# Kernel tuning notes

Measured on AMD Instinct MI355X. Metric: run time of the kernel, lower is better.

Reference implementation:

```python
import jax, jax.numpy as jnp
import numpy as np

NX, NQ, NU = 2048, 2048, 16
EPS = 0.01
STD = 0.5


def setup_inputs() -> dict:
    key = jax.random.key(0)
    ks = jax.random.split(key, 8)
    return {
        "t": 0,
        "x": jax.random.normal(ks[0], (NX,), dtype=jnp.float32),
        "u": jax.random.normal(ks[1], (NU,), dtype=jnp.float32),
        "X": jax.random.normal(ks[2], (NX + NQ, NX + NQ), dtype=jnp.float32) * STD,
        "U": jax.random.normal(ks[3], (NX, NQ), dtype=jnp.float32) * STD,
        "Y1": jax.random.normal(ks[4], (NX, NX), dtype=jnp.float32) * STD,
        "XP": jax.random.normal(ks[5], (NX, NX), dtype=jnp.float32) * STD,
        "B2": jax.random.normal(ks[6], (NX, NU), dtype=jnp.float32) * STD,
        "D12": jax.random.normal(ks[7], (NQ, NU), dtype=jnp.float32) * STD,
    }


def _constrained_mats(X, U, Y1, XP):
    nx = XP.shape[0]
    nq = U.shape[1]
    # P = XP XP^T + eps I ;  H = X X^T + eps I   (F.linear(A,B)=A@B.T)
    P = XP @ XP.T + EPS * jnp.eye(nx, dtype=XP.dtype)
    H = X @ X.T + EPS * jnp.eye(nx + nq, dtype=X.dtype)
    H11 = H[:nx, :nx]
    H12 = H[:nx, nx:]
    H22 = H[nx:, nx:]
    Y = -0.5 * (H11 + Y1 - Y1.T)
    Pinv = jnp.linalg.inv(P)
    A = Pinv @ Y                        # F.linear(inv(P), Y.T) = inv(P) @ Y
    lam = 0.5 * jnp.diagonal(H22)       # diagonal of Lambda
    D11 = -jnp.tril(H22, -1) / lam[:, None]   # strictly lower triangular
    C1 = U.T / lam[:, None]             # inv(Lambda) @ U.T
    B1 = Pinv @ (-H12 - U)
    return A, B1, C1, D11


def _solve_w(D11, c):
    nq = c.shape[0]

    def step(w, inp):
        i, d_row, ci = inp
        wi = jax.nn.relu(ci + jnp.dot(d_row, w))
        return w.at[i].set(wi), None

    w0 = jnp.zeros(nq, dtype=c.dtype)
    w, _ = jax.lax.scan(step, w0, (jnp.arange(nq), D11, c))
    return w


def reference(t, x, u, X, U, Y1, XP, B2, D12):
    A, B1, C1, D11 = _constrained_mats(X, U, Y1, XP)
    c = C1 @ x + D12 @ u                # precomputed affine part (bv = 0, bias=False)
    w = _solve_w(D11, c)
    x_dot = A @ x + B1 @ w + B2 @ u     # bx = 0
    return x_dot
```

## Files before the change

### kernel.cpp

```cpp
#include <hip/hip_runtime.h>
#include <math.h>

#define NQ2 2048
#define NT  4096
#define NUU 16
#define FEPS 0.01f
#define NB  64
#define NBLK 32
#define NSB 128
#define NSP 132
#define NSBLK 16
#define GCH 16

typedef __attribute__((ext_vector_type(8))) short short8;
typedef __attribute__((ext_vector_type(4))) float floatx4;

__device__ __forceinline__ float readlane_f(float v, int lane) {
  return __int_as_float(__builtin_amdgcn_readlane(__float_as_int(v), lane));
}
__device__ __forceinline__ unsigned short f2bf(float x) {
  unsigned u = __float_as_uint(x);
  unsigned r = u + 0x7FFFu + ((u >> 16) & 1u);
  return (unsigned short)(r >> 16);
}
__device__ __forceinline__ float bf2f(unsigned short h) {
  return __uint_as_float(((unsigned)h) << 16);
}

__device__ __forceinline__ float wave_reduce(float v) {
#pragma unroll
  for (int off = 32; off > 0; off >>= 1) v += __shfl_down(v, off, 64);
  return v;
}
__device__ __forceinline__ float block_reduce_256(float v) {
  __shared__ float sm[4];
  v = wave_reduce(v);
  if ((threadIdx.x & 63) == 0) sm[threadIdx.x >> 6] = v;
  __syncthreads();
  return (threadIdx.x == 0) ? (sm[0] + sm[1] + sm[2] + sm[3]) : 0.0f;
}

__global__ __launch_bounds__(256) void lam_kernel(const float* __restrict__ X,
                                                  float* __restrict__ invlam) {
  int row = blockIdx.x;
  const float* xr = X + (size_t)(NQ2 + row) * NT;
  float s = 0.f;
  for (int k = threadIdx.x * 4; k < NT; k += 1024) {
    float4 v = *(const float4*)(xr + k);
    s += v.x * v.x + v.y * v.y + v.z * v.z + v.w * v.w;
  }
  float tot = block_reduce_256(s);
  if (threadIdx.x == 0) invlam[row] = 1.0f / (0.5f * (tot + FEPS));
}

__global__ __launch_bounds__(256) void tgemv_part_kernel(const float* __restrict__ A,
                                                         const float* __restrict__ v,
                                                         float* __restrict__ part) {
  int col = blockIdx.x * 256 + threadIdx.x;
  int ch = blockIdx.y;
  int i0 = ch * (NQ2 / GCH), i1 = i0 + NQ2 / GCH;
  float s = 0.f;
#pragma unroll 4
  for (int i = i0; i < i1; i++) s = fmaf(A[(size_t)i * NQ2 + col], v[i], s);
  part[(size_t)ch * NQ2 + col] = s;
}

template <int FM>
__global__ __launch_bounds__(256) void finish_kernel(const float* __restrict__ part,
                                                     const float* __restrict__ invlam,
                                                     const float* __restrict__ D12,
                                                     const float* __restrict__ u,
                                                     float* __restrict__ dst) {
  int col = blockIdx.x * 256 + threadIdx.x;
  float s = 0.f;
#pragma unroll
  for (int ch = 0; ch < GCH; ch++) s += part[(size_t)ch * NQ2 + col];
  if (FM == 0) {
    float d = 0.f;
#pragma unroll
    for (int j = 0; j < NUU; j++) d += D12[(size_t)col * NUU + j] * u[j];
    dst[col] = s * invlam[col] + d;
  } else if (FM == 1) {
    dst[col] += 0.5f * s;
  } else {
    dst[col] = s;
  }
}

__device__ void syrk512_body(const float* __restrict__ A, int lda, int K,
                             float* __restrict__ C, float eps, int L, int tid) {
  __shared__ __align__(16) short Ah[4096], Al[4096], Bh[4096], Bl[4096];

  int bi = (int)((sqrtf(8.0f * (float)L + 1.0f) - 1.0f) * 0.5f);
  while ((bi + 1) * (bi + 2) / 2 <= L) bi++;
  while (bi * (bi + 1) / 2 > L) bi--;
  int bj = L - bi * (bi + 1) / 2;
  int row0 = bi * 128, col0 = bj * 128;

  int l = tid & 63;
  int w = tid >> 6;
  int wr = w >> 1, wc = w & 1;

  int g = tid;
  int ar = (g >> 6) * 16 + (g & 15), ak = ((g >> 4) & 3) * 8;
  const float* pa = A + (size_t)(row0 + ar) * lda + ak;
  const float* pb = A + (size_t)(col0 + ar) * lda + ak;

  floatx4 acc[4][4];
#pragma unroll
  for (int m = 0; m < 4; m++)
#pragma unroll
    for (int n = 0; n < 4; n++) acc[m][n] = (floatx4){0.f, 0.f, 0.f, 0.f};

  float xa[8], xb[8];
  {
    float4 t0 = *(const float4*)(pa), t1 = *(const float4*)(pa + 4);
    xa[0]=t0.x; xa[1]=t0.y; xa[2]=t0.z; xa[3]=t0.w; xa[4]=t1.x; xa[5]=t1.y; xa[6]=t1.z; xa[7]=t1.w;
    t0 = *(const float4*)(pb); t1 = *(const float4*)(pb + 4);
    xb[0]=t0.x; xb[1]=t0.y; xb[2]=t0.z; xb[3]=t0.w; xb[4]=t1.x; xb[5]=t1.y; xb[6]=t1.z; xb[7]=t1.w;
  }

  for (int k0 = 0; k0 < K; k0 += 32) {
    __syncthreads();
    {
      short8 h, lo;
#pragma unroll
      for (int j = 0; j < 8; j++) { unsigned short hb = f2bf(xa[j]); h[j] = (short)hb; lo[j] = (short)f2bf(xa[j] - bf2f(hb)); }
      *(short8*)&Ah[g * 8] = h; *(short8*)&Al[g * 8] = lo;
#pragma unroll
      for (int j = 0; j < 8; j++) { unsigned short hb = f2bf(xb[j]); h[j] = (short)hb; lo[j] = (short)f2bf(xb[j] - bf2f(hb)); }
      *(short8*)&Bh[g * 8] = h; *(short8*)&Bl[g * 8] = lo;
    }
    __syncthreads();
    if (k0 + 32 < K) {
      const float* q = pa + k0 + 32;
      float4 t0 = *(const float4*)(q), t1 = *(const float4*)(q + 4);
      xa[0]=t0.x; xa[1]=t0.y; xa[2]=t0.z; xa[3]=t0.w; xa[4]=t1.x; xa[5]=t1.y; xa[6]=t1.z; xa[7]=t1.w;
      q = pb + k0 + 32; t0 = *(const float4*)(q); t1 = *(const float4*)(q + 4);
      xb[0]=t0.x; xb[1]=t0.y; xb[2]=t0.z; xb[3]=t0.w; xb[4]=t1.x; xb[5]=t1.y; xb[6]=t1.z; xb[7]=t1.w;
    }
    if (tid < 256) {
      short8 amh[4], aml[4], bnh[4], bnl[4];
#pragma unroll
      for (int m = 0; m < 4; m++) {
        int ga = ((wr * 4 + m) * 64 + l) * 8;
        amh[m] = *(const short8*)&Ah[ga];
        aml[m] = *(const short8*)&Al[ga];
      }
#pragma unroll
      for (int n = 0; n < 4; n++) {
        int gb = ((wc * 4 + n) * 64 + l) * 8;
        bnh[n] = *(const short8*)&Bh[gb];
        bnl[n] = *(const short8*)&Bl[gb];
      }
#pragma unroll
      for (int m = 0; m < 4; m++)
#pragma unroll
        for (int n = 0; n < 4; n++) {
          acc[m][n] = __builtin_amdgcn_mfma_f32_16x16x32_bf16(amh[m], bnh[n], acc[m][n], 0, 0, 0);
          acc[m][n] = __builtin_amdgcn_mfma_f32_16x16x32_bf16(amh[m], bnl[n], acc[m][n], 0, 0, 0);
          acc[m][n] = __builtin_amdgcn_mfma_f32_16x16x32_bf16(aml[m], bnh[n], acc[m][n], 0, 0, 0);
        }
    }
  }

  if (tid < 256) {
    int lr = (l >> 4) * 4;
    int lc = l & 15;
#pragma unroll
    for (int m = 0; m < 4; m++)
#pragma unroll
      for (int n = 0; n < 4; n++)
#pragma unroll
        for (int r = 0; r < 4; r++) {
          int gi = row0 + wr * 64 + m * 16 + lr + r;
          int gj = col0 + wc * 64 + n * 16 + lc;
          float v = acc[m][n][r];
          if (gi == gj) v += eps;
          C[(size_t)gi * NQ2 + gj] = v;
        }
  }
}

__global__ __launch_bounds__(512) void syrk512_kernel(const float* __restrict__ A,
                                                      int lda, int K,
                                                      float* __restrict__ C, float eps) {
  syrk512_body(A, lda, K, C, eps, blockIdx.x, threadIdx.x);
}

__device__ void wsolve_body(const float* __restrict__ M_, const float* __restrict__ rhs,
                            const float* __restrict__ invlam, float* __restrict__ out,
                            int tid) {
  __shared__ float partial[NQ2];
  __shared__ float il[NQ2];
  __shared__ float tile[2][NB][NB + 1];
  __shared__ float vblk[NB];
  int rquad = tid >> 2;
  int l4 = tid & 3;
  for (int i = tid; i < NQ2; i += 512) {
    partial[i] = rhs[i];
    il[i] = invlam[i];
  }
  for (int e = tid; e < NB * NB; e += 512) {
    int rr = e >> 6, cc = e & 63;
    tile[0][rr][cc] = M_[(size_t)rr * NQ2 + cc];
  }
  __syncthreads();
  for (int b = 0; b < NBLK; b++) {
    int cur = b & 1;
    int b0 = b * NB;
    if (tid < 64) {
      int l = tid;
      float creg = partial[b0 + l];
      float ilreg = il[b0 + l];
      float acc = 0.f;
      float wfin = 0.f;
#pragma unroll
      for (int i = 0; i < NB; i++) {
        float cand = fmaxf(creg - acc * ilreg, 0.f);
        float wi = readlane_f(cand, i);
        acc = fmaf(tile[cur][l][i], wi, acc);
        if (l == i) wfin = wi;
      }
      vblk[l] = wfin;
      out[b0 + l] = wfin;
    } else if (b + 1 < NBLK) {
      int b1 = b0 + NB;
      for (int e = tid - 64; e < NB * NB; e += 448) {
        int rr = e >> 6, cc = e & 63;
        tile[cur ^ 1][rr][cc] = M_[(size_t)(b1 + rr) * NQ2 + b1 + cc];
      }
    }
    __syncthreads();
    float4 v0 = *(const float4*)(&vblk[l4 * 16]);
    float4 v1 = *(const float4*)(&vblk[l4 * 16 + 4]);
    float4 v2 = *(const float4*)(&vblk[l4 * 16 + 8]);
    float4 v3 = *(const float4*)(&vblk[l4 * 16 + 12]);
    for (int base = b0 + NB; base < NQ2; base += 512) {
      float accv[4] = {0.f, 0.f, 0.f, 0.f};
#pragma unroll
      for (int rr = 0; rr < 4; rr++) {
        int row = base + rr * 128 + rquad;
        if (row < NQ2) {
          const float* mr = M_ + (size_t)row * NQ2 + b0 + l4 * 16;
          float4 m0 = *(const float4*)(mr);
          float4 m1 = *(const float4*)(mr + 4);
          float4 m2 = *(const float4*)(mr + 8);
          float4 m3 = *(const float4*)(mr + 12);
          accv[rr] = m0.x * v0.x + m0.y * v0.y + m0.z * v0.z + m0.w * v0.w
                   + m1.x * v1.x + m1.y * v1.y + m1.z * v1.z + m1.w * v1.w
                   + m2.x * v2.x + m2.y * v2.y + m2.z * v2.z + m2.w * v2.w
                   + m3.x * v3.x + m3.y * v3.y + m3.z * v3.z + m3.w * v3.w;
        }
      }
#pragma unroll
      for (int rr = 0; rr < 4; rr++) {
        accv[rr] += __shfl_xor(accv[rr], 1);
        accv[rr] += __shfl_xor(accv[rr], 2);
      }
      if (l4 == 0) {
#pragma unroll
        for (int rr = 0; rr < 4; rr++) {
          int row = base + rr * 128 + rquad;
          if (row < NQ2) partial[row] -= accv[rr] * il[row];
        }
      }
    }
    __syncthreads();
  }
}

__global__ __launch_bounds__(512) void wsolve_kernel(const float* __restrict__ M_,
                                                     const float* __restrict__ rhs,
                                                     const float* __restrict__ invlam,
                                                     float* __restrict__ out) {
  wsolve_body(M_, rhs, invlam, out, threadIdx.x);
}

__global__ __launch_bounds__(512) void merged_wsolve_psyrk_kernel(
    const float* __restrict__ Mh22, const float* __restrict__ c,
    const float* __restrict__ invlam, float* __restrict__ w,
    const float* __restrict__ XP, float* __restrict__ P) {
  if (blockIdx.x == 0) {
    wsolve_body(Mh22, c, invlam, w, threadIdx.x);
  } else {
    syrk512_body(XP, NQ2, NQ2, P, FEPS, blockIdx.x - 1, threadIdx.x);
  }
}

__global__ __launch_bounds__(512) void chol_diag128_kernel(float* __restrict__ M_,
                                                           float* __restrict__ Xinvs, int k) {
  __shared__ __align__(16) float Ls[NSB][NSP];
  __shared__ __align__(16) float Xs[NSB][NSP];
  __shared__ float Tmp[32][33];
  __shared__ float dinv[NSB];
  int b0 = k * NSB;
  int tid = threadIdx.x;
  int wv = tid >> 6;
  int lane = tid & 63;

  for (int e = tid; e < NSB * NSP; e += 512) ((float*)Xs)[e] = 0.f;
  for (int e = tid; e < NSB * NSB; e += 512) {
    int rr = e >> 7, cc = e & 127;
    Ls[rr][cc] = M_[(size_t)(b0 + rr) * NQ2 + b0 + cc];
  }
  __syncthreads();

#pragma unroll 1
  for (int kb = 0; kb < 4; kb++) {
    int o = kb * 32;
    if (wv == 0) {
      int r = lane & 31;
      float a[32];
#pragma unroll
      for (int j = 0; j < 32; j++) a[j] = Ls[o + r][o + j];
#pragma unroll
      for (int j = 0; j < 32; j++) {
        float d = readlane_f(a[j], j);
        float rs = rsqrtf(fmaxf(d, 1e-20f));
        a[j] *= rs;
        if (lane == 0) dinv[o + j] = rs;
#pragma unroll
        for (int k2 = j + 1; k2 < 32; k2++) {
          float ljk = readlane_f(a[j], k2);
          a[k2] = fmaf(-a[j], ljk, a[k2]);
        }
      }
      if (lane < 32) {
#pragma unroll
        for (int j = 0; j < 32; j++) Ls[o + r][o + j] = a[j];
      }
    }
    __syncthreads();
    int nrows = 96 - o;
    if (nrows > 0) {
      if (tid < nrows) {
        int r = o + 32 + tid;
        float v[32];
#pragma unroll
        for (int j = 0; j < 32; j++) v[j] = Ls[r][o + j];
#pragma unroll
        for (int t = 0; t < 32; t++) {
          v[t] *= dinv[o + t];
#pragma unroll
          for (int j = t + 1; j < 32; j++)
            v[j] = fmaf(-v[t], Ls[o + j][o + t], v[j]);
        }
#pragma unroll
        for (int j = 0; j < 32; j++) Ls[r][o + j] = v[j];
      }
      __syncthreads();
      int tot = nrows * (nrows + 1) / 2;
      for (int e = tid; e < tot; e += 512) {
        int a = (int)((sqrtf(8.0f * (float)e + 1.0f) - 1.0f) * 0.5f);
        while ((a + 1) * (a + 2) / 2 <= e) a++;
        while (a * (a + 1) / 2 > e) a--;
        int bcol = e - a * (a + 1) / 2;
        int rr = o + 32 + a, cc = o + 32 + bcol;
        float s = 0.f;
#pragma unroll
        for (int t = 0; t < 32; t += 4) {
          float4 av = *(const float4*)&Ls[rr][o + t];
          float4 bv = *(const float4*)&Ls[cc][o + t];
          s += av.x * bv.x + av.y * bv.y + av.z * bv.z + av.w * bv.w;
        }
        Ls[rr][cc] -= s;
      }
      __syncthreads();
    }
  }

  if (wv < 4) {
    int o = wv * 32;
    int c = lane & 31;
    float x[32];
#pragma unroll
    for (int i = 0; i < 32; i++) x[i] = 0.f;
#pragma unroll
    for (int t = 0; t < 32; t++) {
      float rcpd = 1.0f / Ls[o + t][o + t];
      x[t] = (t == c) ? rcpd : x[t] * rcpd;
#pragma unroll
      for (int i = t + 1; i < 32; i++)
        x[i] = fmaf(-Ls[o + i][o + t], x[t], x[i]);
    }
    if (lane < 32) {
#pragma unroll
      for (int i = 0; i < 32; i++) Xs[o + i][o + c] = x[i];
    }
  }
  __syncthreads();

#pragma unroll 1
  for (int j = 0; j < 4; j++) {
#pragma unroll 1
    for (int i = j + 1; i < 4; i++) {
      int oi = i * 32, oj = j * 32;
      for (int e = tid; e < 32 * 32; e += 512) {
        int rr = e >> 5, cc = e & 31;
        float s = 0.f;
        for (int kk = j; kk < i; kk++) {
          int ok = kk * 32;
#pragma unroll
          for (int t = 0; t < 32; t += 4) {
            float4 a = *(const float4*)&Ls[oi + rr][ok + t];
            s += a.x * Xs[ok + t][oj + cc] + a.y * Xs[ok + t + 1][oj + cc]
               + a.z * Xs[ok + t + 2][oj + cc] + a.w * Xs[ok + t + 3][oj + cc];
          }
        }
        Tmp[rr][cc] = s;
      }
      __syncthreads();
      for (int e = tid; e < 32 * 32; e += 512) {
        int rr = e >> 5, cc = e & 31;
        float s = 0.f;
#pragma unroll
        for (int t = 0; t < 32; t += 4) {
          float4 a = *(const float4*)&Xs[oi + rr][oi + t];
          s += a.x * Tmp[t][cc] + a.y * Tmp[t + 1][cc]
             + a.z * Tmp[t + 2][cc] + a.w * Tmp[t + 3][cc];
        }
        Xs[oi + rr][oj + cc] = -s;
      }
      __syncthreads();
    }
  }

  float* Xp = Xinvs + (size_t)k * NSB * NSB;
  for (int e = tid; e < NSB * NSB; e += 512) {
    int rr = e >> 7, cc = e & 127;
    if (cc <= rr) M_[(size_t)(b0 + rr) * NQ2 + b0 + cc] = Ls[rr][cc];
    Xp[e] = Xs[rr][cc];
  }
}

__global__ __launch_bounds__(256) void chol_panel128_kernel(float* __restrict__ M_,
                                                            const float* __restrict__ Xinv,
                                                            int k) {
  int kc = k * NSB;
  int rb0 = kc + NSB + blockIdx.x * 128;
  __shared__ float As[16][128];
  __shared__ float Bs[16][128];
  int tid = threadIdx.x;
  int tx = tid & 15, ty = tid >> 4;
  int sr = tid >> 1, ks = (tid & 1) * 8;

  const float* ap = M_ + (size_t)(rb0 + sr) * NQ2 + kc + ks;
  const float* bp = Xinv + sr * 128 + ks;
  float4 a0 = *(const float4*)(ap), a1 = *(const float4*)(ap + 4);
  float4 b0 = *(const float4*)(bp), b1 = *(const float4*)(bp + 4);

  float acc[8][8] = {{0.f}};
  for (int k0 = 0; k0 < 128; k0 += 16) {
    __syncthreads();
    As[ks + 0][sr] = a0.x; As[ks + 1][sr] = a0.y; As[ks + 2][sr] = a0.z; As[ks + 3][sr] = a0.w;
    As[ks + 4][sr] = a1.x; As[ks + 5][sr] = a1.y; As[ks + 6][sr] = a1.z; As[ks + 7][sr] = a1.w;
    Bs[ks + 0][sr] = b0.x; Bs[ks + 1][sr] = b0.y; Bs[ks + 2][sr] = b0.z; Bs[ks + 3][sr] = b0.w;
    Bs[ks + 4][sr] = b1.x; Bs[ks + 5][sr] = b1.y; Bs[ks + 6][sr] = b1.z; Bs[ks + 7][sr] = b1.w;
    __syncthreads();
    if (k0 + 16 < 128) {
      const float* q = ap + k0 + 16;
      a0 = *(const float4*)(q); a1 = *(const float4*)(q + 4);
      q = bp + k0 + 16;
      b0 = *(const float4*)(q); b1 = *(const float4*)(q + 4);
    }
#pragma unroll
    for (int kk = 0; kk < 16; kk++) {
      float4 aL = *(const float4*)&As[kk][ty * 4];
      float4 aH = *(const float4*)&As[kk][64 + ty * 4];
      float4 bL = *(const float4*)&Bs[kk][tx * 4];
      float4 bH = *(const float4*)&Bs[kk][64 + tx * 4];
      float aa[8] = {aL.x, aL.y, aL.z, aL.w, aH.x, aH.y, aH.z, aH.w};
      float bb[8] = {bL.x, bL.y, bL.z, bL.w, bH.x, bH.y, bH.z, bH.w};
#pragma unroll
      for (int i = 0; i < 8; i++)
#pragma unroll
        for (int j = 0; j < 8; j++) acc[i][j] = fmaf(aa[i], bb[j], acc[i][j]);
    }
  }
#pragma unroll
  for (int ii = 0; ii < 8; ii++) {
    int gi = rb0 + ((ii >> 2) * 64) + ty * 4 + (ii & 3);
#pragma unroll
    for (int half = 0; half < 2; half++) {
      int gj0 = kc + half * 64 + tx * 4;
      float4 o;
      o.x = acc[ii][half * 4 + 0]; o.y = acc[ii][half * 4 + 1];
      o.z = acc[ii][half * 4 + 2]; o.w = acc[ii][half * 4 + 3];
      *(float4*)&M_[(size_t)gi * NQ2 + gj0] = o;
    }
  }
}

__global__ __launch_bounds__(256) void chol_trail128_kernel(float* __restrict__ M_, int k) {
  int L = blockIdx.x;
  int bi = (int)((sqrtf(8.0f * (float)L + 1.0f) - 1.0f) * 0.5f);
  while ((bi + 1) * (bi + 2) / 2 <= L) bi++;
  while (bi * (bi + 1) / 2 > L) bi--;
  int bj = L - bi * (bi + 1) / 2;
  int row0 = (k + 1 + bi) * NSB, col0 = (k + 1 + bj) * NSB, kc = k * NSB;

  __shared__ float As[16][128];
  __shared__ float Bs[16][128];
  int tid = threadIdx.x;
  int tx = tid & 15, ty = tid >> 4;
  int sr = tid >> 1, ks = (tid & 1) * 8;

  const float* ap = M_ + (size_t)(row0 + sr) * NQ2 + kc + ks;
  const float* bp = M_ + (size_t)(col0 + sr) * NQ2 + kc + ks;
  float4 a0 = *(const float4*)(ap), a1 = *(const float4*)(ap + 4);
  float4 b0 = *(const float4*)(bp), b1 = *(const float4*)(bp + 4);

  float acc[8][8] = {{0.f}};
  for (int k0 = 0; k0 < 128; k0 += 16) {
    __syncthreads();
    As[ks + 0][sr] = a0.x; As[ks + 1][sr] = a0.y; As[ks + 2][sr] = a0.z; As[ks + 3][sr] = a0.w;
    As[ks + 4][sr] = a1.x; As[ks + 5][sr] = a1.y; As[ks + 6][sr] = a1.z; As[ks + 7][sr] = a1.w;
    Bs[ks + 0][sr] = b0.x; Bs[ks + 1][sr] = b0.y; Bs[ks + 2][sr] = b0.z; Bs[ks + 3][sr] = b0.w;
    Bs[ks + 4][sr] = b1.x; Bs[ks + 5][sr] = b1.y; Bs[ks + 6][sr] = b1.z; Bs[ks + 7][sr] = b1.w;
    __syncthreads();
    if (k0 + 16 < 128) {
      const float* q = ap + k0 + 16;
      a0 = *(const float4*)(q); a1 = *(const float4*)(q + 4);
      q = bp + k0 + 16;
      b0 = *(const float4*)(q); b1 = *(const float4*)(q + 4);
    }
#pragma unroll
    for (int kk = 0; kk < 16; kk++) {
      float4 aL = *(const float4*)&As[kk][ty * 4];
      float4 aH = *(const float4*)&As[kk][64 + ty * 4];
      float4 bL = *(const float4*)&Bs[kk][tx * 4];
      float4 bH = *(const float4*)&Bs[kk][64 + tx * 4];
      float aa[8] = {aL.x, aL.y, aL.z, aL.w, aH.x, aH.y, aH.z, aH.w};
      float bb[8] = {bL.x, bL.y, bL.z, bL.w, bH.x, bH.y, bH.z, bH.w};
#pragma unroll
      for (int i = 0; i < 8; i++)
#pragma unroll
        for (int j = 0; j < 8; j++) acc[i][j] = fmaf(aa[i], bb[j], acc[i][j]);
    }
  }
#pragma unroll
  for (int ii = 0; ii < 8; ii++) {
    int gi = row0 + ((ii >> 2) * 64) + ty * 4 + (ii & 3);
#pragma unroll
    for (int half = 0; half < 2; half++) {
      int gj0 = col0 + half * 64 + tx * 4;
      float* cp = &M_[(size_t)gi * NQ2 + gj0];
      float4 v = *(const float4*)cp;
      v.x -= acc[ii][half * 4 + 0]; v.y -= acc[ii][half * 4 + 1];
      v.z -= acc[ii][half * 4 + 2]; v.w -= acc[ii][half * 4 + 3];
      *(float4*)cp = v;
    }
  }
}

__global__ __launch_bounds__(1024) void lsolve_kernel(const float* __restrict__ M_,
                                                      const float* __restrict__ Xinvs,
                                                      const float* __restrict__ rhs,
                                                      float* __restrict__ out) {
  __shared__ float partial[NQ2];
  __shared__ float vblk[NSB];
  int tid = threadIdx.x;
  int row8 = tid >> 3, sub = tid & 7;
  for (int i = tid; i < NQ2; i += 1024) partial[i] = rhs[i];
  __syncthreads();
  for (int kb = 0; kb < NSBLK; kb++) {
    int b0 = kb * NSB;
    const float* Xp = Xinvs + (size_t)kb * NSB * NSB;
    {
      int j0 = sub * 16;
      const float* xr = Xp + row8 * NSB + j0;
      float4 x0 = *(const float4*)(xr), x1 = *(const float4*)(xr + 4);
      float4 x2 = *(const float4*)(xr + 8), x3 = *(const float4*)(xr + 12);
      const float* pp = &partial[b0 + j0];
      float s = x0.x*pp[0] + x0.y*pp[1] + x0.z*pp[2] + x0.w*pp[3]
              + x1.x*pp[4] + x1.y*pp[5] + x1.z*pp[6] + x1.w*pp[7]
              + x2.x*pp[8] + x2.y*pp[9] + x2.z*pp[10] + x2.w*pp[11]
              + x3.x*pp[12] + x3.y*pp[13] + x3.z*pp[14] + x3.w*pp[15];
      s += __shfl_xor(s, 1); s += __shfl_xor(s, 2); s += __shfl_xor(s, 4);
      if (sub == 0) { vblk[row8] = s; out[b0 + row8] = s; }
    }
    __syncthreads();
    const float* vp = &vblk[sub * 16];
    for (int base = b0 + NSB; base < NQ2; base += 256) {
      int row0 = base + row8;
      int row1 = row0 + 128;
      float s0 = 0.f, s1 = 0.f;
      if (row0 < NQ2) {
        const float* mr = M_ + (size_t)row0 * NQ2 + b0 + sub * 16;
        float4 m0 = *(const float4*)(mr), m1 = *(const float4*)(mr + 4);
        float4 m2 = *(const float4*)(mr + 8), m3 = *(const float4*)(mr + 12);
        s0 = m0.x*vp[0] + m0.y*vp[1] + m0.z*vp[2] + m0.w*vp[3]
           + m1.x*vp[4] + m1.y*vp[5] + m1.z*vp[6] + m1.w*vp[7]
           + m2.x*vp[8] + m2.y*vp[9] + m2.z*vp[10] + m2.w*vp[11]
           + m3.x*vp[12] + m3.y*vp[13] + m3.z*vp[14] + m3.w*vp[15];
      }
      if (row1 < NQ2) {
        const float* mr = M_ + (size_t)row1 * NQ2 + b0 + sub * 16;
        float4 m0 = *(const float4*)(mr), m1 = *(const float4*)(mr + 4);
        float4 m2 = *(const float4*)(mr + 8), m3 = *(const float4*)(mr + 12);
        s1 = m0.x*vp[0] + m0.y*vp[1] + m0.z*vp[2] + m0.w*vp[3]
           + m1.x*vp[4] + m1.y*vp[5] + m1.z*vp[6] + m1.w*vp[7]
           + m2.x*vp[8] + m2.y*vp[9] + m2.z*vp[10] + m2.w*vp[11]
           + m3.x*vp[12] + m3.y*vp[13] + m3.z*vp[14] + m3.w*vp[15];
      }
      s0 += __shfl_xor(s0, 1); s0 += __shfl_xor(s0, 2); s0 += __shfl_xor(s0, 4);
      s1 += __shfl_xor(s1, 1); s1 += __shfl_xor(s1, 2); s1 += __shfl_xor(s1, 4);
      if (sub == 0) {
        if (row0 < NQ2) partial[row0] -= s0;
        if (row1 < NQ2) partial[row1] -= s1;
      }
    }
    __syncthreads();
  }
}

__global__ __launch_bounds__(1024) void ltsolve_kernel(const float* __restrict__ M_,
                                                       const float* __restrict__ Xinvs,
                                                       const float* __restrict__ rhs,
                                                       float* __restrict__ out) {
  __shared__ float partial[NQ2];
  __shared__ float Xl[NSB][NSB + 1];
  __shared__ float vblk[NSB];
  int tid = threadIdx.x;
  int row8 = tid >> 3, sub = tid & 7;
  for (int i = tid; i < NQ2; i += 1024) partial[i] = rhs[i];
  __syncthreads();
  for (int kb = NSBLK - 1; kb >= 0; kb--) {
    int b0 = kb * NSB;
    const float* Xp = Xinvs + (size_t)kb * NSB * NSB;
    for (int e = tid; e < NSB * NSB; e += 1024) Xl[e >> 7][e & 127] = Xp[e];
    __syncthreads();
    {
      int j0 = sub * 16;
      float s = 0.f;
#pragma unroll
      for (int j = 0; j < 16; j++)
        s = fmaf(Xl[j0 + j][row8], partial[b0 + j0 + j], s);
      s += __shfl_xor(s, 1); s += __shfl_xor(s, 2); s += __shfl_xor(s, 4);
      if (sub == 0) { vblk[row8] = s; out[b0 + row8] = s; }
    }
    __syncthreads();
    for (int i = tid; i < b0; i += 1024) {
      float acc = 0.f;
#pragma unroll 16
      for (int j = 0; j < NSB; j++) acc = fmaf(M_[(size_t)(b0 + j) * NQ2 + i], vblk[j], acc);
      partial[i] -= acc;
    }
    __syncthreads();
  }
}

#define TCH 32
__global__ __launch_bounds__(256) void t_partial_kernel(const float* __restrict__ X,
                                                        const float* __restrict__ x,
                                                        const float* __restrict__ w,
                                                        float* __restrict__ tpart) {
  int k4 = (blockIdx.x * 256 + threadIdx.x) * 4;
  int chunk = blockIdx.y;
  int i0 = chunk * (NT / TCH);
  float4 acc = {0.f, 0.f, 0.f, 0.f};
  for (int i = i0; i < i0 + NT / TCH; i++) {
    float cf = (i < NQ2) ? (-0.5f * x[i]) : (-w[i - NQ2]);
    float4 xv = *(const float4*)(X + (size_t)i * NT + k4);
    acc.x += cf * xv.x; acc.y += cf * xv.y; acc.z += cf * xv.z; acc.w += cf * xv.w;
  }
  *(float4*)(tpart + (size_t)chunk * NT + k4) = acc;
}

__global__ __launch_bounds__(256) void t_reduce_kernel(const float* __restrict__ tpart,
                                                       float* __restrict__ t) {
  int k = blockIdx.x * 256 + threadIdx.x;
  float s = 0.f;
#pragma unroll 8
  for (int ch = 0; ch < TCH; ch++) s += tpart[(size_t)ch * NT + k];
  t[k] = s;
}

__global__ __launch_bounds__(256) void r_kernel(const float* __restrict__ X,
                                                const float* __restrict__ Y1,
                                                const float* __restrict__ U,
                                                const float* __restrict__ t,
                                                const float* __restrict__ x,
                                                const float* __restrict__ w,
                                                float* __restrict__ r) {
  int row = blockIdx.x;
  float s1 = 0.f, s2 = 0.f, s3 = 0.f;
  const float* xr = X + (size_t)row * NT;
  for (int k = threadIdx.x * 4; k < NT; k += 1024) {
    float4 a = *(const float4*)(xr + k);
    float4 b = *(const float4*)(t + k);
    s1 += a.x * b.x + a.y * b.y + a.z * b.z + a.w * b.w;
  }
  const float* yr = Y1 + (size_t)row * NQ2;
  const float* ur = U + (size_t)row * NQ2;
  for (int k = threadIdx.x * 4; k < NQ2; k += 1024) {
    float4 a = *(const float4*)(yr + k);
    float4 b = *(const float4*)(x + k);
    s2 += a.x * b.x + a.y * b.y + a.z * b.z + a.w * b.w;
    float4 c2 = *(const float4*)(ur + k);
    float4 d2 = *(const float4*)(w + k);
    s3 += c2.x * d2.x + c2.y * d2.y + c2.z * d2.z + c2.w * d2.w;
  }
  float v = s1 - 0.5f * s2 - s3;
  float tot = block_reduce_256(v);
  if (threadIdx.x == 0) r[row] = tot - 0.5f * FEPS * x[row];
}

__global__ __launch_bounds__(256) void pz2_res_kernel(const float* __restrict__ XP,
                                                      const float* __restrict__ pz1,
                                                      const float* __restrict__ z,
                                                      const float* __restrict__ r,
                                                      float* __restrict__ res) {
  int row = blockIdx.x;
  float s = 0.f;
  const float* xr = XP + (size_t)row * NQ2;
  for (int k = threadIdx.x * 4; k < NQ2; k += 1024) {
    float4 a = *(const float4*)(xr + k);
    float4 b = *(const float4*)(pz1 + k);
    s += a.x * b.x + a.y * b.y + a.z * b.z + a.w * b.w;
  }
  float tot = block_reduce_256(s);
  if (threadIdx.x == 0) res[row] = r[row] - (tot + FEPS * z[row]);
}

__global__ __launch_bounds__(256) void axpy_kernel(float* __restrict__ z,
                                                   const float* __restrict__ dz) {
  int i = blockIdx.x * 256 + threadIdx.x;
  z[i] += dz[i];
}

__global__ __launch_bounds__(256) void out_kernel(const float* __restrict__ z,
                                                  const float* __restrict__ B2,
                                                  const float* __restrict__ u,
                                                  float* __restrict__ out) {
  int i = blockIdx.x * 256 + threadIdx.x;
  float s = 0.f;
#pragma unroll
  for (int j = 0; j < NUU; j++) s += B2[(size_t)i * NUU + j] * u[j];
  out[i] = z[i] + s;
}

extern "C" void kernel_launch(void* const* d_in, const int* in_sizes, int n_in,
                              void* d_out, int out_size, void* d_ws, size_t ws_size,
                              hipStream_t stream) {
  (void)in_sizes; (void)n_in; (void)out_size;
  const float* x   = (const float*)d_in[1];
  const float* u   = (const float*)d_in[2];
  const float* X   = (const float*)d_in[3];
  const float* U   = (const float*)d_in[4];
  const float* Y1  = (const float*)d_in[5];
  const float* XP  = (const float*)d_in[6];
  const float* B2  = (const float*)d_in[7];
  const float* D12 = (const float*)d_in[8];
  float* out = (float*)d_out;

  float* ws     = (float*)d_ws;
  float* M      = ws;
  float* vecs   = ws + (size_t)NQ2 * NQ2;
  float* invlam = vecs;
  float* c      = vecs + 2048;
  float* w      = vecs + 4096;
  float* r      = vecs + 6144;
  float* y      = vecs + 8192;
  float* z      = vecs + 10240;
  float* dz     = vecs + 12288;
  float* res    = vecs + 14336;
  float* t      = vecs + 16384;
  float* tpart  = vecs + 20480;
  float* gpart  = tpart;
  float* Xinvs  = vecs + 20480 + 32 * 4096;
  float* Ptmp   = Xinvs + (size_t)NSBLK * NSB * NSB;

  size_t need_merged = ((size_t)(Ptmp - ws) + (size_t)NQ2 * NQ2) * sizeof(float);
  bool merged = (ws_size >= need_merged);
  float* P = merged ? Ptmp : M;

  int nsyrk = (NQ2 / 128) * (NQ2 / 128 + 1) / 2;
  dim3 gdim(NQ2 / 256, GCH);
  dim3 tg(4, TCH);

  lam_kernel<<<NQ2, 256, 0, stream>>>(X, invlam);
  tgemv_part_kernel<<<gdim, 256, 0, stream>>>(U, x, gpart);
  finish_kernel<0><<<NQ2 / 256, 256, 0, stream>>>(gpart, invlam, D12, u, c);

  syrk512_kernel<<<nsyrk, 512, 0, stream>>>(X + (size_t)NQ2 * NT, NT, NT, M, 0.0f);

  if (merged) {
    merged_wsolve_psyrk_kernel<<<1 + nsyrk, 512, 0, stream>>>(M, c, invlam, w, XP, Ptmp);
  } else {
    wsolve_kernel<<<1, 512, 0, stream>>>(M, c, invlam, w);
  }

  t_partial_kernel<<<tg, 256, 0, stream>>>(X, x, w, tpart);
  t_reduce_kernel<<<NT / 256, 256, 0, stream>>>(tpart, t);
  r_kernel<<<NQ2, 256, 0, stream>>>(X, Y1, U, t, x, w, r);
  tgemv_part_kernel<<<gdim, 256, 0, stream>>>(Y1, x, gpart);
  finish_kernel<1><<<NQ2 / 256, 256, 0, stream>>>(gpart, invlam, D12, u, r);

  if (!merged) {
    syrk512_kernel<<<nsyrk, 512, 0, stream>>>(XP, NQ2, NQ2, P, FEPS);
  }

  for (int k = 0; k < NSBLK; k++) {
    chol_diag128_kernel<<<1, 512, 0, stream>>>(P, Xinvs, k);
    int rows_below = NQ2 - (k + 1) * NSB;
    if (rows_below > 0) {
      chol_panel128_kernel<<<rows_below / 128, 256, 0, stream>>>(
          P, Xinvs + (size_t)k * NSB * NSB, k);
      int m = NSBLK - 1 - k;
      chol_trail128_kernel<<<m * (m + 1) / 2, 256, 0, stream>>>(P, k);
    }
  }

  lsolve_kernel<<<1, 1024, 0, stream>>>(P, Xinvs, r, y);
  ltsolve_kernel<<<1, 1024, 0, stream>>>(P, Xinvs, y, z);

  {
    tgemv_part_kernel<<<gdim, 256, 0, stream>>>(XP, z, gpart);
    finish_kernel<2><<<NQ2 / 256, 256, 0, stream>>>(gpart, invlam, D12, u, t);
    pz2_res_kernel<<<NQ2, 256, 0, stream>>>(XP, t, z, r, res);
    lsolve_kernel<<<1, 1024, 0, stream>>>(P, Xinvs, res, y);
    ltsolve_kernel<<<1, 1024, 0, stream>>>(P, Xinvs, y, dz);
    axpy_kernel<<<NQ2 / 256, 256, 0, stream>>>(z, dz);
  }

  out_kernel<<<NQ2 / 256, 256, 0, stream>>>(z, B2, u, out);
}
```

Measured before the change: 2.539 ms.

## Overlap next Cholesky diagonal block with trailing update and fuse triangular solves

```diff
diff --git a/kernel.cpp b/kernel.cpp
--- a/kernel.cpp
+++ b/kernel.cpp
@@ -288,14 +288,13 @@
   }
 }
 
-__global__ __launch_bounds__(512) void chol_diag128_kernel(float* __restrict__ M_,
-                                                           float* __restrict__ Xinvs, int k) {
+__device__ void chol_diag128_body(float* __restrict__ M_, float* __restrict__ Xinvs,
+                                  int k, int tid) {
   __shared__ __align__(16) float Ls[NSB][NSP];
   __shared__ __align__(16) float Xs[NSB][NSP];
   __shared__ float Tmp[32][33];
   __shared__ float dinv[NSB];
   int b0 = k * NSB;
-  int tid = threadIdx.x;
   int wv = tid >> 6;
   int lane = tid & 63;
 
@@ -434,6 +433,82 @@
   }
 }
 
+__global__ __launch_bounds__(512) void chol_diag128_kernel(float* __restrict__ M_,
+                                                           float* __restrict__ Xinvs, int k) {
+  chol_diag128_body(M_, Xinvs, k, threadIdx.x);
+}
+
+__device__ void trail512_body(float* __restrict__ M_, int k, int L, int tid) {
+  __shared__ float As[16][128];
+  __shared__ float Bs[16][128];
+  int bi = (int)((sqrtf(8.0f * (float)L + 1.0f) - 1.0f) * 0.5f);
+  while ((bi + 1) * (bi + 2) / 2 <= L) bi++;
+  while (bi * (bi + 1) / 2 > L) bi--;
+  int bj = L - bi * (bi + 1) / 2;
+  int row0 = (k + 1 + bi) * NSB, col0 = (k + 1 + bj) * NSB, kc = k * NSB;
+  const float* ap = M_ + (size_t)row0 * NQ2 + kc;
+  const float* bp = M_ + (size_t)col0 * NQ2 + kc;
+
+  int tx = tid & 15, ty = (tid >> 4) & 15;
+  float acc[8][8] = {{0.f}};
+  for (int k0 = 0; k0 < 128; k0 += 16) {
+    __syncthreads();
+    for (int e = tid; e < 1024; e += 512) {
+      int isB = e >> 9, idx = e & 511;
+      int row = idx >> 2, q = (idx & 3) * 4;
+      const float* src = isB ? bp : ap;
+      float4 v = *(const float4*)(src + (size_t)row * NQ2 + k0 + q);
+      if (isB) { Bs[q][row] = v.x; Bs[q + 1][row] = v.y; Bs[q + 2][row] = v.z; Bs[q + 3][row] = v.w; }
+      else     { As[q][row] = v.x; As[q + 1][row] = v.y; As[q + 2][row] = v.z; As[q + 3][row] = v.w; }
+    }
+    __syncthreads();
+    if (tid < 256) {
+#pragma unroll
+      for (int kk = 0; kk < 16; kk++) {
+        float4 aL = *(const float4*)&As[kk][ty * 4];
+        float4 aH = *(const float4*)&As[kk][64 + ty * 4];
+        float4 bL = *(const float4*)&Bs[kk][tx * 4];
+        float4 bH = *(const float4*)&Bs[kk][64 + tx * 4];
+        float aa[8] = {aL.x, aL.y, aL.z, aL.w, aH.x, aH.y, aH.z, aH.w};
+        float bb[8] = {bL.x, bL.y, bL.z, bL.w, bH.x, bH.y, bH.z, bH.w};
+#pragma unroll
+        for (int i = 0; i < 8; i++)
+#pragma unroll
+          for (int j = 0; j < 8; j++) acc[i][j] = fmaf(aa[i], bb[j], acc[i][j]);
+      }
+    }
+  }
+  if (tid < 256) {
+#pragma unroll
+    for (int ii = 0; ii < 8; ii++) {
+      int gi = row0 + ((ii >> 2) * 64) + ty * 4 + (ii & 3);
+#pragma unroll
+      for (int half = 0; half < 2; half++) {
+        int gj0 = col0 + half * 64 + tx * 4;
+        float* cp = &M_[(size_t)gi * NQ2 + gj0];
+        float4 v = *(const float4*)cp;
+        v.x -= acc[ii][half * 4 + 0]; v.y -= acc[ii][half * 4 + 1];
+        v.z -= acc[ii][half * 4 + 2]; v.w -= acc[ii][half * 4 + 3];
+        *(float4*)cp = v;
+      }
+    }
+  }
+}
+
+__global__ __launch_bounds__(512) void chol_trail_crit_kernel(float* __restrict__ M_, int k) {
+  trail512_body(M_, k, 0, threadIdx.x);
+}
+
+__global__ __launch_bounds__(512) void merged_diag_trail_kernel(float* __restrict__ M_,
+                                                                float* __restrict__ Xinvs,
+                                                                int k) {
+  if (blockIdx.x == 0) {
+    chol_diag128_body(M_, Xinvs, k + 1, threadIdx.x);
+  } else {
+    trail512_body(M_, k, blockIdx.x, threadIdx.x);
+  }
+}
+
 __global__ __launch_bounds__(256) void chol_panel128_kernel(float* __restrict__ M_,
                                                             const float* __restrict__ Xinv,
                                                             int k) {
@@ -492,73 +567,13 @@
   }
 }
 
-__global__ __launch_bounds__(256) void chol_trail128_kernel(float* __restrict__ M_, int k) {
-  int L = blockIdx.x;
-  int bi = (int)((sqrtf(8.0f * (float)L + 1.0f) - 1.0f) * 0.5f);
-  while ((bi + 1) * (bi + 2) / 2 <= L) bi++;
-  while (bi * (bi + 1) / 2 > L) bi--;
-  int bj = L - bi * (bi + 1) / 2;
-  int row0 = (k + 1 + bi) * NSB, col0 = (k + 1 + bj) * NSB, kc = k * NSB;
-
-  __shared__ float As[16][128];
-  __shared__ float Bs[16][128];
-  int tid = threadIdx.x;
-  int tx = tid & 15, ty = tid >> 4;
-  int sr = tid >> 1, ks = (tid & 1) * 8;
-
-  const float* ap = M_ + (size_t)(row0 + sr) * NQ2 + kc + ks;
-  const float* bp = M_ + (size_t)(col0 + sr) * NQ2 + kc + ks;
-  float4 a0 = *(const float4*)(ap), a1 = *(const float4*)(ap + 4);
-  float4 b0 = *(const float4*)(bp), b1 = *(const float4*)(bp + 4);
-
-  float acc[8][8] = {{0.f}};
-  for (int k0 = 0; k0 < 128; k0 += 16) {
-    __syncthreads();
-    As[ks + 0][sr] = a0.x; As[ks + 1][sr] = a0.y; As[ks + 2][sr] = a0.z; As[ks + 3][sr] = a0.w;
-    As[ks + 4][sr] = a1.x; As[ks + 5][sr] = a1.y; As[ks + 6][sr] = a1.z; As[ks + 7][sr] = a1.w;
-    Bs[ks + 0][sr] = b0.x; Bs[ks + 1][sr] = b0.y; Bs[ks + 2][sr] = b0.z; Bs[ks + 3][sr] = b0.w;
-    Bs[ks + 4][sr] = b1.x; Bs[ks + 5][sr] = b1.y; Bs[ks + 6][sr] = b1.z; Bs[ks + 7][sr] = b1.w;
-    __syncthreads();
-    if (k0 + 16 < 128) {
-      const float* q = ap + k0 + 16;
-      a0 = *(const float4*)(q); a1 = *(const float4*)(q + 4);
-      q = bp + k0 + 16;
-      b0 = *(const float4*)(q); b1 = *(const float4*)(q + 4);
-    }
-#pragma unroll
-    for (int kk = 0; kk < 16; kk++) {
-      float4 aL = *(const float4*)&As[kk][ty * 4];
-      float4 aH = *(const float4*)&As[kk][64 + ty * 4];
-      float4 bL = *(const float4*)&Bs[kk][tx * 4];
-      float4 bH = *(const float4*)&Bs[kk][64 + tx * 4];
-      float aa[8] = {aL.x, aL.y, aL.z, aL.w, aH.x, aH.y, aH.z, aH.w};
-      float bb[8] = {bL.x, bL.y, bL.z, bL.w, bH.x, bH.y, bH.z, bH.w};
-#pragma unroll
-      for (int i = 0; i < 8; i++)
-#pragma unroll
-        for (int j = 0; j < 8; j++) acc[i][j] = fmaf(aa[i], bb[j], acc[i][j]);
-    }
-  }
-#pragma unroll
-  for (int ii = 0; ii < 8; ii++) {
-    int gi = row0 + ((ii >> 2) * 64) + ty * 4 + (ii & 3);
-#pragma unroll
-    for (int half = 0; half < 2; half++) {
-      int gj0 = col0 + half * 64 + tx * 4;
-      float* cp = &M_[(size_t)gi * NQ2 + gj0];
-      float4 v = *(const float4*)cp;
-      v.x -= acc[ii][half * 4 + 0]; v.y -= acc[ii][half * 4 + 1];
-      v.z -= acc[ii][half * 4 + 2]; v.w -= acc[ii][half * 4 + 3];
-      *(float4*)cp = v;
-    }
-  }
-}
-
-__global__ __launch_bounds__(1024) void lsolve_kernel(const float* __restrict__ M_,
-                                                      const float* __restrict__ Xinvs,
-                                                      const float* __restrict__ rhs,
-                                                      float* __restrict__ out) {
+__global__ __launch_bounds__(1024) void pchsolve_kernel(const float* __restrict__ M_,
+                                                        const float* __restrict__ Xinvs,
+                                                        const float* __restrict__ rhs,
+                                                        float* __restrict__ out) {
   __shared__ float partial[NQ2];
+  __shared__ float yv[NQ2];
+  __shared__ float Xl[NSB][NSB + 1];
   __shared__ float vblk[NSB];
   int tid = threadIdx.x;
   int row8 = tid >> 3, sub = tid & 7;
@@ -578,7 +593,7 @@
               + x2.x*pp[8] + x2.y*pp[9] + x2.z*pp[10] + x2.w*pp[11]
               + x3.x*pp[12] + x3.y*pp[13] + x3.z*pp[14] + x3.w*pp[15];
       s += __shfl_xor(s, 1); s += __shfl_xor(s, 2); s += __shfl_xor(s, 4);
-      if (sub == 0) { vblk[row8] = s; out[b0 + row8] = s; }
+      if (sub == 0) { vblk[row8] = s; yv[b0 + row8] = s; }
     }
     __syncthreads();
     const float* vp = &vblk[sub * 16];
@@ -613,18 +628,7 @@
     }
     __syncthreads();
   }
-}
-
-__global__ __launch_bounds__(1024) void ltsolve_kernel(const float* __restrict__ M_,
-                                                       const float* __restrict__ Xinvs,
-                                                       const float* __restrict__ rhs,
-                                                       float* __restrict__ out) {
-  __shared__ float partial[NQ2];
-  __shared__ float Xl[NSB][NSB + 1];
-  __shared__ float vblk[NSB];
-  int tid = threadIdx.x;
-  int row8 = tid >> 3, sub = tid & 7;
-  for (int i = tid; i < NQ2; i += 1024) partial[i] = rhs[i];
+  for (int i = tid; i < NQ2; i += 1024) partial[i] = yv[i];
   __syncthreads();
   for (int kb = NSBLK - 1; kb >= 0; kb--) {
     int b0 = kb * NSB;
@@ -762,7 +766,6 @@
   float* c      = vecs + 2048;
   float* w      = vecs + 4096;
   float* r      = vecs + 6144;
-  float* y      = vecs + 8192;
   float* z      = vecs + 10240;
   float* dz     = vecs + 12288;
   float* res    = vecs + 14336;
@@ -802,26 +805,24 @@
     syrk512_kernel<<<nsyrk, 512, 0, stream>>>(XP, NQ2, NQ2, P, FEPS);
   }
 
+  chol_diag128_kernel<<<1, 512, 0, stream>>>(P, Xinvs, 0);
   for (int k = 0; k < NSBLK; k++) {
-    chol_diag128_kernel<<<1, 512, 0, stream>>>(P, Xinvs, k);
-    int rows_below = NQ2 - (k + 1) * NSB;
-    if (rows_below > 0) {
-      chol_panel128_kernel<<<rows_below / 128, 256, 0, stream>>>(
-          P, Xinvs + (size_t)k * NSB * NSB, k);
-      int m = NSBLK - 1 - k;
-      chol_trail128_kernel<<<m * (m + 1) / 2, 256, 0, stream>>>(P, k);
-    }
-  }
-
-  lsolve_kernel<<<1, 1024, 0, stream>>>(P, Xinvs, r, y);
-  ltsolve_kernel<<<1, 1024, 0, stream>>>(P, Xinvs, y, z);
+    int m = NSBLK - 1 - k;
+    if (m > 0) {
+      chol_panel128_kernel<<<m, 256, 0, stream>>>(P, Xinvs + (size_t)k * NSB * NSB, k);
+      chol_trail_crit_kernel<<<1, 512, 0, stream>>>(P, k);
+      int ntiles = m * (m + 1) / 2;
+      merged_diag_trail_kernel<<<ntiles, 512, 0, stream>>>(P, Xinvs, k);
+    }
+  }
+
+  pchsolve_kernel<<<1, 1024, 0, stream>>>(P, Xinvs, r, z);
 
   {
     tgemv_part_kernel<<<gdim, 256, 0, stream>>>(XP, z, gpart);
     finish_kernel<2><<<NQ2 / 256, 256, 0, stream>>>(gpart, invlam, D12, u, t);
     pz2_res_kernel<<<NQ2, 256, 0, stream>>>(XP, t, z, r, res);
-    lsolve_kernel<<<1, 1024, 0, stream>>>(P, Xinvs, res, y);
-    ltsolve_kernel<<<1, 1024, 0, stream>>>(P, Xinvs, y, dz);
+    pchsolve_kernel<<<1, 1024, 0, stream>>>(P, Xinvs, res, dz);
     axpy_kernel<<<NQ2 / 256, 256, 0, stream>>>(z, dz);
   }
 
```

Measured after the change: 2.601 ms. +2.5%, slower.
